# Performance work log

Hardware: AMD Instinct MI355X
Metric: run time of the kernel (lower is better)

Reference implementation:

```python
import jax, jax.numpy as jnp
import numpy as np

N = 50000      # nodes
E = 400000     # edges (avg degree 8)
F_IN = 128     # input feature dim
H = 4          # heads (layer 1)
D = 128        # hidden per head
C = 3          # classes (layer 2 out, 1 head)
EPS = 1e-5     # BatchNorm eps
SLOPE = 0.2    # LeakyReLU negative slope (DGL GATConv default)


def setup_inputs() -> dict:
    key = jax.random.key(0)
    ks = jax.random.split(key, 16)
    s = jnp.float32(0.05)
    return {
        "features": jax.random.normal(ks[0], (N, F_IN), jnp.float32),
        "src": jax.random.randint(ks[1], (E,), 0, N, jnp.int32),
        "dst": jax.random.randint(ks[2], (E,), 0, N, jnp.int32),
        # GATConv layer 1 params
        "W1": jax.random.normal(ks[3], (F_IN, H * D), jnp.float32) * s,
        "al1": jax.random.normal(ks[4], (H, D), jnp.float32) * s,
        "ar1": jax.random.normal(ks[5], (H, D), jnp.float32) * s,
        "b1": jnp.zeros((H * D,), jnp.float32),
        "Wres1": jax.random.normal(ks[6], (F_IN, H * D), jnp.float32) * s,
        # BatchNorm1d (inference mode)
        "bn_gamma": jnp.ones((H * D,), jnp.float32),
        "bn_beta": jnp.zeros((H * D,), jnp.float32),
        "bn_mean": jnp.zeros((H * D,), jnp.float32),
        "bn_var": jnp.ones((H * D,), jnp.float32),
        # GATConv layer 2 params (1 head, C out)
        "W2": jax.random.normal(ks[7], (H * D, C), jnp.float32) * s,
        "al2": jax.random.normal(ks[8], (1, C), jnp.float32) * s,
        "ar2": jax.random.normal(ks[9], (1, C), jnp.float32) * s,
        "b2": jnp.zeros((C,), jnp.float32),
        "Wres2": jax.random.normal(ks[10], (H * D, C), jnp.float32) * s,
    }


def _gat_layer(x, src, dst, W, attn_l, attn_r, bias, Wres, heads, dim):
    """DGL GATConv (eval mode): gather, LeakyReLU score, segment softmax,
    weighted scatter-sum, linear residual, bias."""
    n = x.shape[0]
    z = (x @ W).reshape(n, heads, dim)                 # [N,H,D]
    el = jnp.sum(z * attn_l, axis=-1)                  # [N,H]
    er = jnp.sum(z * attn_r, axis=-1)                  # [N,H]
    e = jax.nn.leaky_relu(el[src] + er[dst], SLOPE)    # [E,H]
    # segment softmax over incoming edges of each dst node
    m = jax.ops.segment_max(e, dst, num_segments=n)    # [N,H]
    ex = jnp.exp(e - m[dst])                           # [E,H]
    den = jax.ops.segment_sum(ex, dst, num_segments=n) # [N,H]
    alpha = ex / den[dst]                              # [E,H]
    # weighted message aggregation
    rst = jax.ops.segment_sum(z[src] * alpha[..., None], dst, num_segments=n)  # [N,H,D]
    res = (x @ Wres).reshape(n, heads, dim)
    return rst + res + bias.reshape(1, heads, dim)


def reference(features, src, dst, W1, al1, ar1, b1, Wres1,
              bn_gamma, bn_beta, bn_mean, bn_var,
              W2, al2, ar2, b2, Wres2):
    h = _gat_layer(features, src, dst, W1, al1, ar1, b1, Wres1, H, D)
    h = h.reshape(N, H * D)
    # BatchNorm1d (inference) + ELU; dropout is identity in eval mode
    h = (h - bn_mean) * jax.lax.rsqrt(bn_var + EPS) * bn_gamma + bn_beta
    h = jax.nn.elu(h)
    h = _gat_layer(h, src, dst, W2, al2, ar2, b2, Wres2, 1, C)
    return h[:, 0, :]  # squeeze head dim -> [N, C]
```

## Files before the change

kernel.cpp:

```cpp
#include <hip/hip_runtime.h>
#include <hip/hip_bf16.h>

#define N_NODES 50000
#define N_EDGES 400000
#define FIN     128
#define HD      512
#define SLOPE   0.2f
#define NB_X    782

typedef __hip_bfloat16 bf16;
typedef __bf16 bf16x8 __attribute__((ext_vector_type(8)));
typedef __bf16 bf16x4 __attribute__((ext_vector_type(4)));
typedef __bf16 bf16x2 __attribute__((ext_vector_type(2)));
typedef float  f32x4  __attribute__((ext_vector_type(4)));
typedef float  f32x2  __attribute__((ext_vector_type(2)));

__global__ void sentinel_k(float* out, int n) {
    int i = blockIdx.x * 256 + threadIdx.x;
    if (i < n) out[i] = 12288.0f;
}

__global__ __launch_bounds__(256) void prep_k(const float* __restrict__ W1, const float* __restrict__ Wres1,
                                              const float* __restrict__ al1, const float* __restrict__ ar1,
                                              const float* __restrict__ W2, const float* __restrict__ Wres2,
                                              const float* __restrict__ b1,
                                              const float* __restrict__ bnm, const float* __restrict__ bnv,
                                              const float* __restrict__ bng, const float* __restrict__ bnb,
                                              bf16* __restrict__ Wfrag, float* __restrict__ tab,
                                              bf16* __restrict__ wlrb,
                                              int* __restrict__ deg, int* __restrict__ cur0) {
    int b = blockIdx.x;
    if (b < 196) {
        int i = b * 256 + threadIdx.x;
        if (i < N_NODES) { deg[i] = 0; cur0[i] = 0; }
        return;
    }
    b -= 196;
    if (b < 64) {
        int f = b * 256 + threadIdx.x;
        int lane = f & 63, unit = f >> 6;
        int tile = unit >> 3, ks = unit & 7;
        int cl = lane & 15, rg = lane >> 4;
        int gc = tile * 16 + cl;
        int k0 = ks * 32 + rg * 8;
        bf16x8 v;
#pragma unroll
        for (int j = 0; j < 8; ++j) {
            int kk = k0 + j;
            float x = (kk < 128) ? W1[kk * HD + gc] : Wres1[(kk - 128) * HD + gc];
            v[j] = (__bf16)x;
        }
        *reinterpret_cast<bf16x8*>(reinterpret_cast<char*>(Wfrag) + (size_t)f * 16) = v;
        return;
    }
    b -= 64;
    if (b < 16) {
        int i = b * 256 + threadIdx.x;
        int gc = i >> 3, c = i & 7;
        float v;
        if (c < 2) {
            float rs = rsqrtf(bnv[gc] + 1e-5f) * bng[gc];
            v = (c == 0) ? rs : (b1[gc] - bnm[gc]) * rs + bnb[gc];
        } else if (c < 5) {
            v = W2[gc * 3 + (c - 2)];
        } else {
            v = Wres2[gc * 3 + (c - 5)];
        }
        tab[i] = v;
        return;
    }
    for (int i = 0; i < 8; ++i) {
        int e = i * 256 + threadIdx.x;
        int ks = e >> 9, lane = (e >> 3) & 63, j = e & 7;
        int r = lane & 15, rg = lane >> 4;
        int k = ks * 32 + rg * 8 + j;
        float v = 0.f;
        if (r < 4) {
            for (int d = 0; d < 128; ++d) v += W1[k * HD + r * 128 + d] * al1[r * 128 + d];
        } else if (r < 8) {
            int h = r - 4;
            for (int d = 0; d < 128; ++d) v += W1[k * HD + h * 128 + d] * ar1[h * 128 + d];
        }
        wlrb[e] = __float2bfloat16(v);
    }
}

__global__ __launch_bounds__(256) void eler_k(const float* __restrict__ X,
                                              const bf16* __restrict__ wlrb,
                                              float* __restrict__ el, float* __restrict__ er,
                                              bf16* __restrict__ Xb,
                                              const int* __restrict__ dst, int* __restrict__ deg) {
    if (blockIdx.x >= NB_X) {
        int e = (blockIdx.x - NB_X) * 256 + threadIdx.x;
        if (e < N_EDGES) atomicAdd(&deg[dst[e]], 1);
        return;
    }
    __shared__ __align__(16) char XSb[64 * 256];
    const int t = threadIdx.x;
    const int w = t >> 6, lane = t & 63;
    const int cl = lane & 15, rg = lane >> 4;
    const int m0 = blockIdx.x * 64;

#pragma unroll
    for (int j = 0; j < 8; ++j) {
        int e = j * 1024 + t * 4;
        int row = e >> 7, col = e & 127;
        int grow = m0 + row;
        int gc = grow < N_NODES ? grow : N_NODES - 1;
        f32x4 v = *reinterpret_cast<const f32x4*>(X + (size_t)gc * FIN + col);
        bf16x4 bv = {(__bf16)v[0], (__bf16)v[1], (__bf16)v[2], (__bf16)v[3]};
        if (grow < N_NODES)
            *reinterpret_cast<bf16x4*>(Xb + (size_t)grow * FIN + col) = bv;
        int byte = (row * 256 + col * 2) ^ ((row & 7) << 4);
        *reinterpret_cast<bf16x4*>(XSb + byte) = bv;
    }
    __syncthreads();

    f32x4 a = {0.f, 0.f, 0.f, 0.f};
    const int row = w * 16 + cl;
    const int swz = (row & 7) << 4;
#pragma unroll
    for (int ks = 0; ks < 4; ++ks) {
        bf16x8 af = *reinterpret_cast<const bf16x8*>(
            reinterpret_cast<const char*>(wlrb) + ((size_t)(ks * 64 + lane)) * 16);
        int byte = (row * 256 + ks * 64 + rg * 16) ^ swz;
        bf16x8 bf = *reinterpret_cast<const bf16x8*>(XSb + byte);
        a = __builtin_amdgcn_mfma_f32_16x16x32_bf16(af, bf, a, 0, 0, 0);
    }
    int n = m0 + row;
    if (n < N_NODES) {
        if (rg == 0)      *reinterpret_cast<float4*>(el + (size_t)n * 4) = make_float4(a[0], a[1], a[2], a[3]);
        else if (rg == 1) *reinterpret_cast<float4*>(er + (size_t)n * 4) = make_float4(a[0], a[1], a[2], a[3]);
    }
}

__global__ __launch_bounds__(256) void scan1_k(const int* __restrict__ deg,
                                               int* __restrict__ rloc, int* __restrict__ blksum) {
    __shared__ int wsum[4];
    int t = threadIdx.x, b = blockIdx.x;
    int i = b * 256 + t;
    int v = (i < N_NODES) ? deg[i] : 0;
    int lane = t & 63, w = t >> 6;
    int x = v;
#pragma unroll
    for (int off = 1; off < 64; off <<= 1) {
        int y = __shfl_up(x, off);
        if (lane >= off) x += y;
    }
    if (lane == 63) wsum[w] = x;
    __syncthreads();
    int wadd = 0;
    if (w > 0) wadd += wsum[0];
    if (w > 1) wadd += wsum[1];
    if (w > 2) wadd += wsum[2];
    int incl = x + wadd;
    if (i < N_NODES) rloc[i] = incl - v;
    if (t == 255) blksum[b] = incl;
}

__global__ __launch_bounds__(256) void scan2_k(int* __restrict__ blksum) {
    __shared__ int wsum[4];
    int t = threadIdx.x;
    int v = (t < 196) ? blksum[t] : 0;
    int lane = t & 63, w = t >> 6;
    int x = v;
#pragma unroll
    for (int off = 1; off < 64; off <<= 1) {
        int y = __shfl_up(x, off);
        if (lane >= off) x += y;
    }
    if (lane == 63) wsum[w] = x;
    __syncthreads();
    int wadd = 0;
    if (w > 0) wadd += wsum[0];
    if (w > 1) wadd += wsum[1];
    if (w > 2) wadd += wsum[2];
    if (t < 196) blksum[t] = x + wadd - v;
}

__global__ void fill_k(const int* __restrict__ src, const int* __restrict__ dst,
                       const int* __restrict__ rloc, const int* __restrict__ bsum,
                       int* __restrict__ cur0, int* __restrict__ csr) {
    int e = blockIdx.x * 256 + threadIdx.x;
    if (e < N_EDGES) {
        int d = dst[e];
        int slot = atomicAdd(&cur0[d], 1);
        csr[rloc[d] + bsum[d >> 8] + slot] = src[e];
    }
}

__global__ __launch_bounds__(1024) void aggX_k(const int* __restrict__ rloc, const int* __restrict__ bsum,
                                               const int* __restrict__ degA, const int* __restrict__ csr,
                                               const float* __restrict__ el, const float* __restrict__ er,
                                               const bf16* __restrict__ Xb, bf16* __restrict__ AGGb,
                                               float* __restrict__ den4) {
    __shared__ int    ssrc[16][64];
    __shared__ float4 spe4[16][64];

    const int w = threadIdx.x >> 6, lane = threadIdx.x & 63;
    const int sub = lane >> 5, ll = lane & 31;
    const int n = blockIdx.x * 16 + w;
    const int beg = rloc[n] + bsum[n >> 8];
    const int deg = degA[n];
    const float4 ern = *reinterpret_cast<const float4*>(er + (size_t)n * 4);
    const char* Xbc = reinterpret_cast<const char*>(Xb);

    f32x2 accA[4] = {{0.f,0.f},{0.f,0.f},{0.f,0.f},{0.f,0.f}};
    f32x2 accB[4] = {{0.f,0.f},{0.f,0.f},{0.f,0.f},{0.f,0.f}};
    float dreg = 0.f;

    for (int base = 0; base < deg; base += 64) {
        const int cnt = min(64, deg - base);
        if (lane < cnt) {
            int s = csr[beg + base + lane];
            ssrc[w][lane] = s;
            float4 e4 = *reinterpret_cast<const float4*>(el + (size_t)s * 4);
            float4 p; float e;
            e = e4.x + ern.x; e = e > 0.f ? e : SLOPE * e; p.x = __expf(e);
            e = e4.y + ern.y; e = e > 0.f ? e : SLOPE * e; p.y = __expf(e);
            e = e4.z + ern.z; e = e > 0.f ? e : SLOPE * e; p.z = __expf(e);
            e = e4.w + ern.w; e = e > 0.f ? e : SLOPE * e; p.w = __expf(e);
            spe4[w][lane] = p;
        }
        asm volatile("s_waitcnt lgkmcnt(0)" ::: "memory");
        if (lane < 4) {
            for (int j = 0; j < cnt; ++j)
                dreg += reinterpret_cast<const float*>(&spe4[w][j])[lane];
        }
        for (int jj = 0; jj < cnt; jj += 2) {
            int j2 = jj + sub;
            int jc = j2 < cnt ? j2 : cnt - 1;
            int s = ssrc[w][jc];
            uint2 xv = *reinterpret_cast<const uint2*>(Xbc + (size_t)s * 256 + ll * 8);
            float4 p = spe4[w][jc];
            if (j2 >= cnt) p = make_float4(0.f, 0.f, 0.f, 0.f);
            f32x2 xlo = {__uint_as_float(xv.x << 16), __uint_as_float(xv.x & 0xffff0000u)};
            f32x2 xhi = {__uint_as_float(xv.y << 16), __uint_as_float(xv.y & 0xffff0000u)};
            accA[0] += p.x * xlo; accB[0] += p.x * xhi;
            accA[1] += p.y * xlo; accB[1] += p.y * xhi;
            accA[2] += p.z * xlo; accB[2] += p.z * xhi;
            accA[3] += p.w * xlo; accB[3] += p.w * xhi;
        }
        asm volatile("s_waitcnt lgkmcnt(0)" ::: "memory");
    }

#pragma unroll
    for (int h = 0; h < 4; ++h) {
        accA[h][0] += __shfl_xor(accA[h][0], 32);
        accA[h][1] += __shfl_xor(accA[h][1], 32);
        accB[h][0] += __shfl_xor(accB[h][0], 32);
        accB[h][1] += __shfl_xor(accB[h][1], 32);
    }
    if (sub == 0) {
#pragma unroll
        for (int h = 0; h < 4; ++h) {
            bf16x4 v = {(__bf16)accA[h][0], (__bf16)accA[h][1],
                        (__bf16)accB[h][0], (__bf16)accB[h][1]};
            *reinterpret_cast<bf16x4*>(AGGb + (size_t)n * 512 + h * 128 + ll * 4) = v;
        }
    }
    if (lane < 4) den4[(size_t)n * 4 + lane] = dreg;
}

__global__ __launch_bounds__(256) void gemm2_k(
    const bf16* __restrict__ Xb, const bf16* __restrict__ AGGb,
    const float* __restrict__ den4,
    const bf16* __restrict__ Wfrag, const float* __restrict__ tab,
    const float* __restrict__ al2, const float* __restrict__ ar2,
    float* __restrict__ node2) {
    __shared__ __align__(16) char XS[32 * 256];
    __shared__ __align__(16) char AGS[32 * 1024];
    __shared__ float zsum[4][32][6];

    const int t = threadIdx.x;
    const int w = t >> 6, lane = t & 63;
    const int cl = lane & 15, rg = lane >> 4;
    const int m0 = blockIdx.x * 32;

#pragma unroll
    for (int j = 0; j < 2; ++j) {
        int L = j * 4096 + t * 16;
        int row = L >> 8, col = L & 255;
        int grow = m0 + row; grow = grow < N_NODES ? grow : N_NODES - 1;
        bf16x8 v = *reinterpret_cast<const bf16x8*>(
            reinterpret_cast<const char*>(Xb) + (size_t)grow * 256 + col);
        int byte = (row * 256 + col) ^ ((row & 7) << 4);
        *reinterpret_cast<bf16x8*>(XS + byte) = v;
    }
#pragma unroll
    for (int j = 0; j < 8; ++j) {
        int L = j * 4096 + t * 16;
        int row = L >> 10, col = L & 1023;
        int grow = m0 + row; grow = grow < N_NODES ? grow : N_NODES - 1;
        bf16x8 v = *reinterpret_cast<const bf16x8*>(
            reinterpret_cast<const char*>(AGGb) + (size_t)grow * 1024 + col);
        int byte = (row * 1024 + col) ^ ((row & 7) << 4);
        *reinterpret_cast<bf16x8*>(AGS + byte) = v;
    }
    __syncthreads();

    float invden[2];
#pragma unroll
    for (int mt = 0; mt < 2; ++mt) {
        int nn = m0 + mt * 16 + cl;
        nn = nn < N_NODES ? nn : N_NODES - 1;
        float d = den4[(size_t)nn * 4 + w];
        invden[mt] = d > 0.f ? 1.f / d : 0.f;
    }

    float z2p[2][3] = {}, r2p[2][3] = {};

#pragma unroll
    for (int ct = 0; ct < 8; ++ct) {
        const int unit = (w * 8 + ct) * 8;
        bf16x8 af[8];
#pragma unroll
        for (int ks = 0; ks < 8; ++ks)
            af[ks] = *reinterpret_cast<const bf16x8*>(
                reinterpret_cast<const char*>(Wfrag) + ((size_t)(unit + ks) * 64 + lane) * 16);
        const int gcl = w * 128 + ct * 16 + rg * 4;
        f32x4 t0[4], t1[4];
#pragma unroll
        for (int i = 0; i < 4; ++i) {
            t0[i] = *reinterpret_cast<const f32x4*>(tab + (size_t)(gcl + i) * 8);
            t1[i] = *reinterpret_cast<const f32x4*>(tab + (size_t)(gcl + i) * 8 + 4);
        }
#pragma unroll
        for (int mt = 0; mt < 2; ++mt) {
            int row = mt * 16 + cl;
            int swz = (row & 7) << 4;
            f32x4 aA = {0.f, 0.f, 0.f, 0.f};
            f32x4 aX = {0.f, 0.f, 0.f, 0.f};
#pragma unroll
            for (int ks = 0; ks < 4; ++ks) {
                int byte = (row * 1024 + w * 256 + ks * 64 + rg * 16) ^ swz;
                bf16x8 bfr = *reinterpret_cast<const bf16x8*>(AGS + byte);
                aA = __builtin_amdgcn_mfma_f32_16x16x32_bf16(af[ks], bfr, aA, 0, 0, 0);
            }
#pragma unroll
            for (int ks = 0; ks < 4; ++ks) {
                int byte = (row * 256 + ks * 64 + rg * 16) ^ swz;
                bf16x8 bfr = *reinterpret_cast<const bf16x8*>(XS + byte);
                aX = __builtin_amdgcn_mfma_f32_16x16x32_bf16(af[ks + 4], bfr, aX, 0, 0, 0);
            }
#pragma unroll
            for (int i = 0; i < 4; ++i) {
                float z = aA[i] * invden[mt] + aX[i];
                float hv = z * t0[i][0] + t0[i][1];
                hv = hv > 0.f ? hv : (__expf(hv) - 1.f);
                z2p[mt][0] += hv * t0[i][2]; z2p[mt][1] += hv * t0[i][3]; z2p[mt][2] += hv * t1[i][0];
                r2p[mt][0] += hv * t1[i][1]; r2p[mt][1] += hv * t1[i][2]; r2p[mt][2] += hv * t1[i][3];
            }
        }
    }

#pragma unroll
    for (int mt = 0; mt < 2; ++mt)
#pragma unroll
        for (int c = 0; c < 3; ++c) {
            z2p[mt][c] += __shfl_xor(z2p[mt][c], 16);
            z2p[mt][c] += __shfl_xor(z2p[mt][c], 32);
            r2p[mt][c] += __shfl_xor(r2p[mt][c], 16);
            r2p[mt][c] += __shfl_xor(r2p[mt][c], 32);
        }
    if (rg == 0) {
#pragma unroll
        for (int mt = 0; mt < 2; ++mt) {
            int nl = mt * 16 + cl;
            zsum[w][nl][0] = z2p[mt][0]; zsum[w][nl][1] = z2p[mt][1]; zsum[w][nl][2] = z2p[mt][2];
            zsum[w][nl][3] = r2p[mt][0]; zsum[w][nl][4] = r2p[mt][1]; zsum[w][nl][5] = r2p[mt][2];
        }
    }
    __syncthreads();
    if (t < 32) {
        float v[6];
#pragma unroll
        for (int c = 0; c < 6; ++c)
            v[c] = zsum[0][t][c] + zsum[1][t][c] + zsum[2][t][c] + zsum[3][t][c];
        int n = m0 + t;
        if (n < N_NODES) {
            float e2l = v[0] * al2[0] + v[1] * al2[1] + v[2] * al2[2];
            float e2r = v[0] * ar2[0] + v[1] * ar2[1] + v[2] * ar2[2];
            *reinterpret_cast<float4*>(node2 + (size_t)n * 8) = make_float4(v[0], v[1], v[2], e2l);
            *reinterpret_cast<float4*>(node2 + (size_t)n * 8 + 4) = make_float4(v[3], v[4], v[5], e2r);
        }
    }
}

__global__ __launch_bounds__(256) void agg2_k(const int* __restrict__ rloc, const int* __restrict__ bsum,
                                              const int* __restrict__ degA, const int* __restrict__ csr,
                                              const float* __restrict__ node2,
                                              const float* __restrict__ b2, float* __restrict__ out) {
    int wv = threadIdx.x >> 6, lane = threadIdx.x & 63;
    int n = blockIdx.x * 4 + wv;
    int beg = rloc[n] + bsum[n >> 8];
    int deg = degA[n];
    float ern = node2[(size_t)n * 8 + 7];
    float den = 0.f, a0 = 0.f, a1 = 0.f, a2 = 0.f;
    for (int j = lane; j < deg; j += 64) {
        int s = csr[beg + j];
        float4 v = *reinterpret_cast<const float4*>(node2 + (size_t)s * 8);
        float e = v.w + ern;
        e = e > 0.f ? e : SLOPE * e;
        float p = __expf(e);
        den += p;
        a0 += p * v.x; a1 += p * v.y; a2 += p * v.z;
    }
#pragma unroll
    for (int off = 32; off > 0; off >>= 1) {
        den += __shfl_xor(den, off);
        a0 += __shfl_xor(a0, off); a1 += __shfl_xor(a1, off); a2 += __shfl_xor(a2, off);
    }
    if (lane == 0) {
        float inv = deg > 0 ? 1.f / den : 0.f;
        float4 r = *reinterpret_cast<const float4*>(node2 + (size_t)n * 8 + 4);
        out[(size_t)n * 3 + 0] = a0 * inv + r.x + b2[0];
        out[(size_t)n * 3 + 1] = a1 * inv + r.y + b2[1];
        out[(size_t)n * 3 + 2] = a2 * inv + r.z + b2[2];
    }
}

extern "C" void kernel_launch(void* const* d_in, const int* in_sizes, int n_in,
                              void* d_out, int out_size, void* d_ws, size_t ws_size,
                              hipStream_t stream) {
    const float* X     = (const float*)d_in[0];
    const int*   src   = (const int*)d_in[1];
    const int*   dst   = (const int*)d_in[2];
    const float* W1    = (const float*)d_in[3];
    const float* al1   = (const float*)d_in[4];
    const float* ar1   = (const float*)d_in[5];
    const float* b1    = (const float*)d_in[6];
    const float* Wres1 = (const float*)d_in[7];
    const float* bng   = (const float*)d_in[8];
    const float* bnb   = (const float*)d_in[9];
    const float* bnm   = (const float*)d_in[10];
    const float* bnv   = (const float*)d_in[11];
    const float* W2    = (const float*)d_in[12];
    const float* al2   = (const float*)d_in[13];
    const float* ar2   = (const float*)d_in[14];
    const float* b2    = (const float*)d_in[15];
    const float* Wres2 = (const float*)d_in[16];
    float* out = (float*)d_out;

    char* p = (char*)d_ws;
    auto carve = [&](size_t bytes) -> char* {
        char* r = p;
        p += (bytes + 255) & ~(size_t)255;
        return r;
    };
    bf16*  Wfrag  = (bf16*)carve((size_t)512 * 256 * 2);
    float* tab    = (float*)carve((size_t)512 * 8 * 4);
    bf16*  wlrb   = (bf16*)carve((size_t)2048 * 2);
    float* el     = (float*)carve((size_t)N_NODES * 4 * 4);
    float* er     = (float*)carve((size_t)N_NODES * 4 * 4);
    int*   deg    = (int*)carve((size_t)N_NODES * 4);
    int*   rloc   = (int*)carve((size_t)(N_NODES + 256) * 4);
    int*   cur0   = (int*)carve((size_t)N_NODES * 4);
    int*   bsum   = (int*)carve((size_t)256 * 4);
    int*   csr    = (int*)carve((size_t)N_EDGES * 4);
    bf16*  Xb     = (bf16*)carve((size_t)N_NODES * FIN * 2);
    bf16*  AGGb   = (bf16*)carve((size_t)N_NODES * 512 * 2);
    float* den4   = (float*)carve((size_t)(N_NODES + 64) * 4 * 4);
    float* node2  = (float*)carve((size_t)N_NODES * 8 * 4);
    size_t need = (size_t)(p - (char*)d_ws);
    if (need > ws_size) {
        sentinel_k<<<(out_size + 255) / 256, 256, 0, stream>>>(out, out_size);
        return;
    }

    prep_k<<<196 + 64 + 16 + 1, 256, 0, stream>>>(W1, Wres1, al1, ar1, W2, Wres2, b1,
                                                  bnm, bnv, bng, bnb, Wfrag, tab, wlrb, deg, cur0);
    eler_k<<<NB_X + (N_EDGES + 255) / 256, 256, 0, stream>>>(X, wlrb, el, er, Xb, dst, deg);
    scan1_k<<<196, 256, 0, stream>>>(deg, rloc, bsum);
    scan2_k<<<1, 256, 0, stream>>>(bsum);
    fill_k<<<(N_EDGES + 255) / 256, 256, 0, stream>>>(src, dst, rloc, bsum, cur0, csr);
    aggX_k<<<N_NODES / 16, 1024, 0, stream>>>(rloc, bsum, deg, csr, el, er, Xb, AGGb, den4);
    gemm2_k<<<(N_NODES + 31) / 32, 256, 0, stream>>>(Xb, AGGb, den4, Wfrag, tab, al2, ar2, node2);
    agg2_k<<<N_NODES / 4, 256, 0, stream>>>(rloc, bsum, deg, csr, node2, b2, out);
}
```

Measured before the change: 183.6 us.

## Assign one node per half-wave in layer-1 aggregation, broadcast edges via shuffles

The aggregation kernel now maps each 32-lane half-wavefront to its own destination node instead of one node per wavefront, doubling nodes per block and removing the cross-half reduction. Edge source indices and attention exponentials are computed per lane and broadcast with wave shuffles rather than staged through shared memory with explicit waits. The intent is to cut idle lanes on low-degree nodes and remove LDS traffic and synchronization. In exchange, the two halves of a wavefront can diverge when their nodes have different degrees, and each edge now costs five shuffles.

```diff
diff --git a/kernel.cpp b/kernel.cpp
--- a/kernel.cpp
+++ b/kernel.cpp
@@ -194,12 +194,11 @@
                                                const float* __restrict__ el, const float* __restrict__ er,
                                                const bf16* __restrict__ Xb, bf16* __restrict__ AGGb,
                                                float* __restrict__ den4) {
-    __shared__ int    ssrc[16][64];
-    __shared__ float4 spe4[16][64];
-
     const int w = threadIdx.x >> 6, lane = threadIdx.x & 63;
     const int sub = lane >> 5, ll = lane & 31;
-    const int n = blockIdx.x * 16 + w;
+    int n = blockIdx.x * 32 + w * 2 + sub;
+    const bool valid = n < N_NODES;
+    if (!valid) n = N_NODES - 1;
     const int beg = rloc[n] + bsum[n >> 8];
     const int deg = degA[n];
     const float4 ern = *reinterpret_cast<const float4*>(er + (size_t)n * 4);
@@ -207,59 +206,47 @@
 
     f32x2 accA[4] = {{0.f,0.f},{0.f,0.f},{0.f,0.f},{0.f,0.f}};
     f32x2 accB[4] = {{0.f,0.f},{0.f,0.f},{0.f,0.f},{0.f,0.f}};
-    float dreg = 0.f;
-
-    for (int base = 0; base < deg; base += 64) {
-        const int cnt = min(64, deg - base);
-        if (lane < cnt) {
-            int s = csr[beg + base + lane];
-            ssrc[w][lane] = s;
-            float4 e4 = *reinterpret_cast<const float4*>(el + (size_t)s * 4);
-            float4 p; float e;
-            e = e4.x + ern.x; e = e > 0.f ? e : SLOPE * e; p.x = __expf(e);
-            e = e4.y + ern.y; e = e > 0.f ? e : SLOPE * e; p.y = __expf(e);
-            e = e4.z + ern.z; e = e > 0.f ? e : SLOPE * e; p.z = __expf(e);
-            e = e4.w + ern.w; e = e > 0.f ? e : SLOPE * e; p.w = __expf(e);
-            spe4[w][lane] = p;
-        }
-        asm volatile("s_waitcnt lgkmcnt(0)" ::: "memory");
-        if (lane < 4) {
-            for (int j = 0; j < cnt; ++j)
-                dreg += reinterpret_cast<const float*>(&spe4[w][j])[lane];
-        }
-        for (int jj = 0; jj < cnt; jj += 2) {
-            int j2 = jj + sub;
-            int jc = j2 < cnt ? j2 : cnt - 1;
-            int s = ssrc[w][jc];
-            uint2 xv = *reinterpret_cast<const uint2*>(Xbc + (size_t)s * 256 + ll * 8);
-            float4 p = spe4[w][jc];
-            if (j2 >= cnt) p = make_float4(0.f, 0.f, 0.f, 0.f);
+    float4 dp = make_float4(0.f, 0.f, 0.f, 0.f);
+
+    for (int base = 0; base < deg; base += 32) {
+        const int cnt = min(32, deg - base);
+        int s = 0;
+        if (ll < cnt) s = csr[beg + base + ll];
+        float4 e4 = *reinterpret_cast<const float4*>(el + (size_t)s * 4);
+        float4 p; float e;
+        e = e4.x + ern.x; e = e > 0.f ? e : SLOPE * e; p.x = __expf(e);
+        e = e4.y + ern.y; e = e > 0.f ? e : SLOPE * e; p.y = __expf(e);
+        e = e4.z + ern.z; e = e > 0.f ? e : SLOPE * e; p.z = __expf(e);
+        e = e4.w + ern.w; e = e > 0.f ? e : SLOPE * e; p.w = __expf(e);
+
+        for (int j = 0; j < cnt; ++j) {
+            int idx = sub * 32 + j;
+            int sj = __shfl(s, idx);
+            uint2 xv = *reinterpret_cast<const uint2*>(Xbc + (size_t)sj * 256 + ll * 8);
+            float4 pj;
+            pj.x = __shfl(p.x, idx);
+            pj.y = __shfl(p.y, idx);
+            pj.z = __shfl(p.z, idx);
+            pj.w = __shfl(p.w, idx);
+            dp.x += pj.x; dp.y += pj.y; dp.z += pj.z; dp.w += pj.w;
             f32x2 xlo = {__uint_as_float(xv.x << 16), __uint_as_float(xv.x & 0xffff0000u)};
             f32x2 xhi = {__uint_as_float(xv.y << 16), __uint_as_float(xv.y & 0xffff0000u)};
-            accA[0] += p.x * xlo; accB[0] += p.x * xhi;
-            accA[1] += p.y * xlo; accB[1] += p.y * xhi;
-            accA[2] += p.z * xlo; accB[2] += p.z * xhi;
-            accA[3] += p.w * xlo; accB[3] += p.w * xhi;
-        }
-        asm volatile("s_waitcnt lgkmcnt(0)" ::: "memory");
-    }
-
-#pragma unroll
-    for (int h = 0; h < 4; ++h) {
-        accA[h][0] += __shfl_xor(accA[h][0], 32);
-        accA[h][1] += __shfl_xor(accA[h][1], 32);
-        accB[h][0] += __shfl_xor(accB[h][0], 32);
-        accB[h][1] += __shfl_xor(accB[h][1], 32);
-    }
-    if (sub == 0) {
+            accA[0] += pj.x * xlo; accB[0] += pj.x * xhi;
+            accA[1] += pj.y * xlo; accB[1] += pj.y * xhi;
+            accA[2] += pj.z * xlo; accB[2] += pj.z * xhi;
+            accA[3] += pj.w * xlo; accB[3] += pj.w * xhi;
+        }
+    }
+
+    if (valid) {
 #pragma unroll
         for (int h = 0; h < 4; ++h) {
             bf16x4 v = {(__bf16)accA[h][0], (__bf16)accA[h][1],
                         (__bf16)accB[h][0], (__bf16)accB[h][1]};
             *reinterpret_cast<bf16x4*>(AGGb + (size_t)n * 512 + h * 128 + ll * 4) = v;
         }
-    }
-    if (lane < 4) den4[(size_t)n * 4 + lane] = dreg;
+        if (ll == 0) *reinterpret_cast<float4*>(den4 + (size_t)n * 4) = dp;
+    }
 }
 
 __global__ __launch_bounds__(256) void gemm2_k(
@@ -474,7 +461,7 @@
     scan1_k<<<196, 256, 0, stream>>>(deg, rloc, bsum);
     scan2_k<<<1, 256, 0, stream>>>(bsum);
     fill_k<<<(N_EDGES + 255) / 256, 256, 0, stream>>>(src, dst, rloc, bsum, cur0, csr);
-    aggX_k<<<N_NODES / 16, 1024, 0, stream>>>(rloc, bsum, deg, csr, el, er, Xb, AGGb, den4);
+    aggX_k<<<(N_NODES + 31) / 32, 1024, 0, stream>>>(rloc, bsum, deg, csr, el, er, Xb, AGGb, den4);
     gemm2_k<<<(N_NODES + 31) / 32, 256, 0, stream>>>(Xb, AGGb, den4, Wfrag, tab, al2, ar2, node2);
     agg2_k<<<N_NODES / 4, 256, 0, stream>>>(rloc, bsum, deg, csr, node2, b2, out);
 }
```

After: 176.6 us. -3.8%, faster.
